# Optimization experiments

Hardware: AMD Instinct MI355X
Metric: run time of the kernel (lower is better)

The kernel has to match this reference:

```python
import jax, jax.numpy as jnp
import numpy as np

HEAD = 8
PAD = (2, 2)   # (mod//2, mod//2 + mod%2) for dim=508, head=8 -> mod=4
EPS = 1e-6


def setup_inputs() -> dict:
    key = jax.random.key(0)
    ks = jax.random.split(key, 4)
    d_pad = 512  # 508 + mod(4)
    s = 1.0 / np.sqrt(d_pad).astype(np.float32)
    inp = jax.random.normal(ks[0], (2, 2048, 508), dtype=jnp.float32)
    Wq = jax.random.normal(ks[1], (d_pad, d_pad), dtype=jnp.float32) * s
    Wk = jax.random.normal(ks[2], (d_pad, d_pad), dtype=jnp.float32) * s
    Wv = jax.random.normal(ks[3], (d_pad, d_pad), dtype=jnp.float32) * s
    gamma = jnp.ones((d_pad,), dtype=jnp.float32)
    beta = jnp.zeros((d_pad,), dtype=jnp.float32)
    return {"inp": inp, "Wq": Wq, "Wk": Wk, "Wv": Wv, "gamma": gamma, "beta": beta}


def reference(inp, Wq, Wk, Wv, gamma, beta):
    # pad feature dim so it divides head count (torch F.pad on last dim)
    x = jnp.pad(inp, ((0, 0), (0, 0), (PAD[0], PAD[1])))  # [B, L, D]
    residual = x
    b, l, d = x.shape
    h = HEAD
    dh = d // h
    inv_sqrt_dh = 1.0 / np.sqrt(dh).astype(np.float32)

    def proj(W):
        # torch Linear (no bias): x @ W.T ; then split heads -> [B, H, L, dh]
        return (x @ W.T).reshape(b, l, h, dh).transpose(0, 2, 1, 3)

    q = proj(Wq)
    k = proj(Wk)
    v = proj(Wv)

    score = jnp.einsum('bhld,bhmd->bhlm', q, k) * inv_sqrt_dh  # [B,H,L,L]
    attn = jax.nn.softmax(score, axis=-1)
    out = jnp.einsum('bhlm,bhmd->bhld', attn, v)               # [B,H,L,dh]
    out = out.transpose(0, 2, 1, 3).reshape(b, l, d)           # unshape

    # dropout is identity in eval mode; residual + layernorm
    y = out + residual
    mu = jnp.mean(y, axis=-1, keepdims=True)
    var = jnp.mean(jnp.square(y - mu), axis=-1, keepdims=True)
    z = (y - mu) / jnp.sqrt(var + EPS)
    out = gamma * z + beta

    out = out[:, :, PAD[0]:-PAD[1]]  # strip padding back to original dim
    return out, attn
```

## Files before the change

kernel.cpp:

```cpp
#include <hip/hip_runtime.h>

typedef short bf16x8 __attribute__((ext_vector_type(8)));
typedef float f32x4 __attribute__((ext_vector_type(4)));
typedef unsigned short u16;
typedef u16 u16x8 __attribute__((ext_vector_type(8)));
typedef u16 u16x4 __attribute__((ext_vector_type(4)));

#define L_ 2048
#define D_ 512
#define H_ 8
#define DH_ 64
#define DIN 508

static __device__ __forceinline__ u16 f2b(float f){
  unsigned u = __builtin_bit_cast(unsigned, f);
  unsigned r = u + 0x7fffu + ((u >> 16) & 1u);
  return (u16)(r >> 16);
}
static __device__ __forceinline__ float b2f(u16 u){
  unsigned x = ((unsigned)u) << 16;
  return __builtin_bit_cast(float, x);
}
#define MFMA16(a,b,c) __builtin_amdgcn_mfma_f32_16x16x32_bf16(a,b,c,0,0,0)

__global__ __launch_bounds__(512) void cvt_kernel(
    const float* __restrict__ inp, const float* __restrict__ Wq,
    const float* __restrict__ Wk, const float* __restrict__ Wv,
    u16* __restrict__ Xb, u16* __restrict__ Wb)
{
  const int tid = blockIdx.x*512 + threadIdx.x;
  if (tid < 262144) {
    const int idx8 = tid*8;
    const int row = idx8 >> 9, col = idx8 & 511;
    u16x8 o;
    #pragma unroll
    for (int e=0;e<8;++e){
      const int c = col+e;
      const float v = (c>=2 && c<510) ? inp[(size_t)row*DIN + (c-2)] : 0.f;
      o[e] = f2b(v);
    }
    *(u16x8*)&Xb[idx8] = o;
  } else {
    const int idx8 = (tid - 262144)*8;
    const int row = idx8 >> 9, col = idx8 & 511;
    const float* __restrict__ W = (row < 512) ? Wq : (row < 1024) ? Wk : Wv;
    const float* p = &W[(size_t)(row & 511)*D_ + col];
    u16x8 o;
    #pragma unroll
    for (int e=0;e<8;++e) o[e] = f2b(p[e]);
    *(u16x8*)&Wb[idx8] = o;
  }
}

__global__ __launch_bounds__(512) void proj_kernel(
    const u16* __restrict__ Xb, const u16* __restrict__ Wb,
    u16* __restrict__ Qg, u16* __restrict__ Kg, u16* __restrict__ Vt)
{
  __shared__ u16 Xl[128*72];
  __shared__ u16 Wl[128*72];
  const int t = threadIdx.x;
  const int lane = t & 63, wid = t >> 6;
  const int wr = wid >> 2, wc = wid & 3;
  const int i0 = blockIdx.x * 128;
  const int j0 = blockIdx.y * 128;
  const int mat = j0 >> 9;
  const int srow = t >> 3, sc8 = (t & 7) * 8;

  f32x4 acc[4][2];
  #pragma unroll
  for (int a=0;a<4;++a){
    #pragma unroll
    for (int bq=0;bq<2;++bq){ f32x4 z = {0.f,0.f,0.f,0.f}; acc[a][bq] = z; }
  }

  u16x8 xa0 = *(const u16x8*)&Xb[(size_t)(i0+srow)*D_ + sc8];
  u16x8 xa1 = *(const u16x8*)&Xb[(size_t)(i0+64+srow)*D_ + sc8];
  u16x8 wa0 = *(const u16x8*)&Wb[(size_t)(j0+srow)*D_ + sc8];
  u16x8 wa1 = *(const u16x8*)&Wb[(size_t)(j0+64+srow)*D_ + sc8];

  for (int kt=0; kt<8; ++kt){
    __syncthreads();
    *(u16x8*)&Xl[srow*72 + sc8] = xa0;
    *(u16x8*)&Xl[(64+srow)*72 + sc8] = xa1;
    *(u16x8*)&Wl[srow*72 + sc8] = wa0;
    *(u16x8*)&Wl[(64+srow)*72 + sc8] = wa1;
    __syncthreads();
    if (kt < 7){
      const int k1 = (kt+1)*64;
      xa0 = *(const u16x8*)&Xb[(size_t)(i0+srow)*D_ + k1 + sc8];
      xa1 = *(const u16x8*)&Xb[(size_t)(i0+64+srow)*D_ + k1 + sc8];
      wa0 = *(const u16x8*)&Wb[(size_t)(j0+srow)*D_ + k1 + sc8];
      wa1 = *(const u16x8*)&Wb[(size_t)(j0+64+srow)*D_ + k1 + sc8];
    }
    #pragma unroll
    for (int ks=0; ks<2; ++ks){
      const int ko = ks*32 + (lane>>4)*8;
      bf16x8 af[4], bfr[2];
      #pragma unroll
      for (int fm=0; fm<4; ++fm)
        af[fm] = *(const bf16x8*)&Xl[(wr*64 + fm*16 + (lane&15))*72 + ko];
      #pragma unroll
      for (int fn=0; fn<2; ++fn)
        bfr[fn] = *(const bf16x8*)&Wl[(wc*32 + fn*16 + (lane&15))*72 + ko];
      #pragma unroll
      for (int fm=0; fm<4; ++fm){
        #pragma unroll
        for (int fn=0; fn<2; ++fn)
          acc[fm][fn] = MFMA16(af[fm], bfr[fn], acc[fm][fn]);
      }
    }
  }
  #pragma unroll
  for (int fm=0; fm<4; ++fm){
    const int ibase = i0 + wr*64 + fm*16 + (lane>>4)*4;
    const int b = ibase >> 11;
    const int li = ibase & (L_-1);
    #pragma unroll
    for (int fn=0; fn<2; ++fn){
      const int n = j0 + wc*32 + fn*16 + (lane&15);
      const int h = (n>>6) & 7;
      const int dh = n & 63;
      if (mat == 2){
        u16x4 pk;
        #pragma unroll
        for (int r=0;r<4;++r) pk[r] = f2b(acc[fm][fn][r]);
        *(u16x4*)&Vt[((size_t)(b*H_+h)*DH_ + dh)*L_ + li] = pk;
      } else {
        u16* dst = ((mat==0)? Qg : Kg) + ((size_t)(b*H_+h)*L_ + li)*DH_ + dh;
        #pragma unroll
        for (int r=0;r<4;++r) dst[(size_t)r*DH_] = f2b(acc[fm][fn][r]);
      }
    }
  }
}

__global__ __launch_bounds__(512, 4) void attn_kernel(
    const u16* __restrict__ Qg, const u16* __restrict__ Kg,
    const u16* __restrict__ Vt, float* __restrict__ attn, float* __restrict__ Og)
{
  __shared__ u16 Kl[128*72];
  __shared__ u16 Vl[64*136];
  __shared__ u16 Pt[32*136];
  __shared__ float rsp[8][32];
  __shared__ float inv_rs[32];

  const int t = threadIdx.x, lane = t & 63, wid = t >> 6;
  const int lin = blockIdx.x;
  const int idx = lin >> 3;
  const int bh = (lin & 7) + 8*(idx & 1);
  const int q0 = (idx >> 1) * 32;
  const u16* Qp = Qg + ((size_t)bh*L_ + q0)*DH_;
  const u16* Kp = Kg + (size_t)bh*L_*DH_;
  const u16* Vp = Vt + (size_t)bh*DH_*L_;

  bf16x8 qf[2][2];
  #pragma unroll
  for (int qi=0;qi<2;++qi){
    #pragma unroll
    for (int ks=0;ks<2;++ks)
      qf[qi][ks] = *(const bf16x8*)&Qp[(size_t)(qi*16 + (lane&15))*DH_ + ks*32 + (lane>>4)*8];
  }

  const int kr0 = t>>3, kc8 = (t&7)*8;
  const int vr0 = t>>4, vcm = (t&15)*8;
  const int g4 = (lane>>4)*8;
  const int mrow = wid*16 + (lane&15);

  float racc0 = 0.f, racc1 = 0.f;
  u16x8 ka = *(const u16x8*)&Kp[(size_t)kr0*DH_ + kc8];
  u16x8 kb = *(const u16x8*)&Kp[(size_t)(64+kr0)*DH_ + kc8];
  for (int kt=0; kt<16; ++kt){
    __syncthreads();
    *(u16x8*)&Kl[kr0*72 + kc8] = ka;
    *(u16x8*)&Kl[(64+kr0)*72 + kc8] = kb;
    __syncthreads();
    if (kt < 15){
      ka = *(const u16x8*)&Kp[(size_t)((kt+1)*128 + kr0)*DH_ + kc8];
      kb = *(const u16x8*)&Kp[(size_t)((kt+1)*128 + 64 + kr0)*DH_ + kc8];
    }
    bf16x8 kf0 = *(const bf16x8*)&Kl[mrow*72 + g4];
    bf16x8 kf1 = *(const bf16x8*)&Kl[mrow*72 + 32 + g4];
    f32x4 s0 = {0.f,0.f,0.f,0.f}, s1 = {0.f,0.f,0.f,0.f};
    s0 = MFMA16(kf0, qf[0][0], s0); s0 = MFMA16(kf1, qf[0][1], s0);
    s1 = MFMA16(kf0, qf[1][0], s1); s1 = MFMA16(kf1, qf[1][1], s1);
    #pragma unroll
    for (int r=0;r<4;++r){
      racc0 += __expf(s0[r]*0.125f);
      racc1 += __expf(s1[r]*0.125f);
    }
  }
  racc0 += __shfl_xor(racc0, 16); racc0 += __shfl_xor(racc0, 32);
  racc1 += __shfl_xor(racc1, 16); racc1 += __shfl_xor(racc1, 32);
  if (lane < 16){ rsp[wid][lane] = racc0; rsp[wid][16+lane] = racc1; }
  __syncthreads();
  if (t < 32){
    float s = 0.f;
    #pragma unroll
    for (int w=0;w<8;++w) s += rsp[w][t];
    inv_rs[t] = 1.f/s;
  }
  __syncthreads();

  const int qpv = wid>>2, d0 = (wid&3)*16;
  f32x4 o0 = {0.f,0.f,0.f,0.f}, o1 = {0.f,0.f,0.f,0.f};
  const int sr = t >> 4;
  const int sc4 = (t & 15) * 4;
  float* abase = attn + ((size_t)bh*L_ + q0 + sr)*L_ + sc4;
  const float sinv = inv_rs[sr];

  ka = *(const u16x8*)&Kp[(size_t)kr0*DH_ + kc8];
  kb = *(const u16x8*)&Kp[(size_t)(64+kr0)*DH_ + kc8];
  u16x8 va = *(const u16x8*)&Vp[(size_t)vr0*L_ + vcm];
  u16x8 vb = *(const u16x8*)&Vp[(size_t)(32+vr0)*L_ + vcm];
  for (int kt=0; kt<16; ++kt){
    __syncthreads();
    *(u16x8*)&Kl[kr0*72 + kc8] = ka;
    *(u16x8*)&Kl[(64+kr0)*72 + kc8] = kb;
    *(u16x8*)&Vl[vr0*136 + vcm] = va;
    *(u16x8*)&Vl[(32+vr0)*136 + vcm] = vb;
    __syncthreads();
    if (kt < 15){
      ka = *(const u16x8*)&Kp[(size_t)((kt+1)*128 + kr0)*DH_ + kc8];
      kb = *(const u16x8*)&Kp[(size_t)((kt+1)*128 + 64 + kr0)*DH_ + kc8];
      va = *(const u16x8*)&Vp[(size_t)vr0*L_ + (kt+1)*128 + vcm];
      vb = *(const u16x8*)&Vp[(size_t)(32+vr0)*L_ + (kt+1)*128 + vcm];
    }
    bf16x8 kf0 = *(const bf16x8*)&Kl[mrow*72 + g4];
    bf16x8 kf1 = *(const bf16x8*)&Kl[mrow*72 + 32 + g4];
    f32x4 s0 = {0.f,0.f,0.f,0.f}, s1 = {0.f,0.f,0.f,0.f};
    s0 = MFMA16(kf0, qf[0][0], s0); s0 = MFMA16(kf1, qf[0][1], s0);
    s1 = MFMA16(kf0, qf[1][0], s1); s1 = MFMA16(kf1, qf[1][1], s1);
    u16x4 p0, p1;
    p0[0] = f2b(__expf(s0[0]*0.125f)); p0[1] = f2b(__expf(s0[1]*0.125f));
    p0[2] = f2b(__expf(s0[2]*0.125f)); p0[3] = f2b(__expf(s0[3]*0.125f));
    p1[0] = f2b(__expf(s1[0]*0.125f)); p1[1] = f2b(__expf(s1[1]*0.125f));
    p1[2] = f2b(__expf(s1[2]*0.125f)); p1[3] = f2b(__expf(s1[3]*0.125f));
    *(u16x4*)&Pt[(lane&15)*136 + wid*16 + (lane>>4)*4] = p0;
    *(u16x4*)&Pt[(16 + (lane&15))*136 + wid*16 + (lane>>4)*4] = p1;
    __syncthreads();
    {
      const u16x4 pva = *(const u16x4*)&Pt[sr*136 + sc4];
      const u16x4 pvb = *(const u16x4*)&Pt[sr*136 + 64 + sc4];
      f32x4 w0, w1;
      w0[0]=b2f(pva[0])*sinv; w0[1]=b2f(pva[1])*sinv;
      w0[2]=b2f(pva[2])*sinv; w0[3]=b2f(pva[3])*sinv;
      w1[0]=b2f(pvb[0])*sinv; w1[1]=b2f(pvb[1])*sinv;
      w1[2]=b2f(pvb[2])*sinv; w1[3]=b2f(pvb[3])*sinv;
      __builtin_nontemporal_store(w0, (f32x4*)&abase[kt*128]);
      __builtin_nontemporal_store(w1, (f32x4*)&abase[kt*128 + 64]);
    }
    #pragma unroll
    for (int ms=0; ms<4; ++ms){
      bf16x8 pa = *(const bf16x8*)&Pt[(qpv*16 + (lane&15))*136 + ms*32 + g4];
      bf16x8 vv = *(const bf16x8*)&Vl[(d0 + (lane&15))*136 + ms*32 + g4];
      if (ms&1) o1 = MFMA16(pa, vv, o1); else o0 = MFMA16(pa, vv, o0);
    }
  }
  {
    const int b = bh>>3, h = bh&7;
    #pragma unroll
    for (int r=0;r<4;++r){
      const int qr = qpv*16 + (lane>>4)*4 + r;
      Og[((size_t)(b*L_ + q0 + qr))*D_ + h*DH_ + d0 + (lane&15)] = (o0[r]+o1[r])*inv_rs[qr];
    }
  }
}

__global__ __launch_bounds__(256) void ln_kernel(
    const float* __restrict__ Og, const float* __restrict__ inp,
    const float* __restrict__ gamma, const float* __restrict__ beta,
    float* __restrict__ out0)
{
  const int row = blockIdx.x, t = threadIdx.x;
  const int lane = t & 63, wid = t >> 6;
  const int c2 = t + 256;
  const float x1 = (t >= 2) ? inp[(size_t)row*DIN + t-2] : 0.f;
  const float x2 = (c2 < 510) ? inp[(size_t)row*DIN + c2-2] : 0.f;
  const float y1 = Og[(size_t)row*D_ + t]  + x1;
  const float y2 = Og[(size_t)row*D_ + c2] + x2;
  float s = y1 + y2, ss = y1*y1 + y2*y2;
  #pragma unroll
  for (int off=1; off<64; off<<=1){
    s  += __shfl_xor(s,  off);
    ss += __shfl_xor(ss, off);
  }
  __shared__ float red[4][2];
  if (lane == 0){ red[wid][0] = s; red[wid][1] = ss; }
  __syncthreads();
  s  = red[0][0]+red[1][0]+red[2][0]+red[3][0];
  ss = red[0][1]+red[1][1]+red[2][1]+red[3][1];
  const float mu   = s * (1.f/512.f);
  const float var  = ss * (1.f/512.f) - mu*mu;
  const float rstd = rsqrtf(var + 1e-6f);
  const float z1 = (y1 - mu)*rstd*gamma[t]  + beta[t];
  const float z2 = (y2 - mu)*rstd*gamma[c2] + beta[c2];
  if (t >= 2)   out0[(size_t)row*DIN + t-2]  = z1;
  if (c2 < 510) out0[(size_t)row*DIN + c2-2] = z2;
}

extern "C" void kernel_launch(void* const* d_in, const int* in_sizes, int n_in,
                              void* d_out, int out_size, void* d_ws, size_t ws_size,
                              hipStream_t stream) {
  const float* inp   = (const float*)d_in[0];
  const float* Wq    = (const float*)d_in[1];
  const float* Wk    = (const float*)d_in[2];
  const float* Wv    = (const float*)d_in[3];
  const float* gamma = (const float*)d_in[4];
  const float* beta  = (const float*)d_in[5];

  char* ws = (char*)d_ws;
  u16*   Qg = (u16*)(ws);
  u16*   Kg = (u16*)(ws + 4194304);
  u16*   Vt = (u16*)(ws + 8388608);
  float* Og = (float*)(ws + 12582912);
  u16*   Xb = (u16*)(ws + 12582912);
  u16*   Wb = (u16*)(ws + 16777216);

  float* out0 = (float*)d_out;
  float* attn = out0 + 2080768;

  cvt_kernel <<<704, 512, 0, stream>>>(inp, Wq, Wk, Wv, Xb, Wb);
  proj_kernel<<<dim3(32,12), 512, 0, stream>>>(Xb, Wb, Qg, Kg, Vt);
  attn_kernel<<<1024, 512, 0, stream>>>(Qg, Kg, Vt, attn, Og);
  ln_kernel  <<<4096, 256, 0, stream>>>(Og, inp, gamma, beta, out0);
}
```

Before: 127.1 us.

## Load K/V fragments straight from global, compute PV in registers, double-buffer P

The attention kernel stops staging K and V through shared memory. Each wave loads its K rows and V^T fragments directly from global memory and feeds them to MFMA. PV is now computed per wave with 16x16x16 MFMAs on the wave's own P fragment, so the P tile no longer needs a round trip through LDS before the PV product, and two syncs per iteration are removed. P is double-buffered in LDS only for writing out the attention matrix. Each wave then holds partial outputs for all 32x64 elements, which must be tree-reduced across 8 waves through shared memory at the end. This raises register pressure and redundant global traffic for V, which each wave reads for its own key slice.

```diff
diff --git a/kernel.cpp b/kernel.cpp
--- a/kernel.cpp
+++ b/kernel.cpp
@@ -1,6 +1,7 @@
 #include <hip/hip_runtime.h>
 
 typedef short bf16x8 __attribute__((ext_vector_type(8)));
+typedef short bf16x4 __attribute__((ext_vector_type(4)));
 typedef float f32x4 __attribute__((ext_vector_type(4)));
 typedef unsigned short u16;
 typedef u16 u16x8 __attribute__((ext_vector_type(8)));
@@ -21,7 +22,30 @@
   unsigned x = ((unsigned)u) << 16;
   return __builtin_bit_cast(float, x);
 }
+static __device__ __forceinline__ bf16x8 asbf(u16x8 v){
+  return __builtin_bit_cast(bf16x8, v);
+}
+static __device__ __forceinline__ bf16x4 asbf4(u16x4 v){
+  return __builtin_bit_cast(bf16x4, v);
+}
 #define MFMA16(a,b,c) __builtin_amdgcn_mfma_f32_16x16x32_bf16(a,b,c,0,0,0)
+
+#if __has_builtin(__builtin_amdgcn_mfma_f32_16x16x16bf16_1k)
+static __device__ __forceinline__ f32x4 MFMA16K16(bf16x4 a, bf16x4 b, f32x4 c){
+  return __builtin_amdgcn_mfma_f32_16x16x16bf16_1k(a, b, c, 0, 0, 0);
+}
+#elif __has_builtin(__builtin_amdgcn_mfma_f32_16x16x16_bf16)
+static __device__ __forceinline__ f32x4 MFMA16K16(bf16x4 a, bf16x4 b, f32x4 c){
+  return __builtin_amdgcn_mfma_f32_16x16x16_bf16(a, b, c, 0, 0, 0);
+}
+#else
+static __device__ __forceinline__ f32x4 MFMA16K16(bf16x4 a, bf16x4 b, f32x4 c){
+  f32x4 d;
+  asm volatile("v_mfma_f32_16x16x16_bf16 %0, %1, %2, %3\n\ts_nop 7"
+               : "=&v"(d) : "v"(a), "v"(b), "v"(c));
+  return d;
+}
+#endif
 
 __global__ __launch_bounds__(512) void cvt_kernel(
     const float* __restrict__ inp, const float* __restrict__ Wq,
@@ -138,13 +162,15 @@
     const u16* __restrict__ Qg, const u16* __restrict__ Kg,
     const u16* __restrict__ Vt, float* __restrict__ attn, float* __restrict__ Og)
 {
-  __shared__ u16 Kl[128*72];
-  __shared__ u16 Vl[64*136];
-  __shared__ u16 Pt[32*136];
-  __shared__ float rsp[8][32];
-  __shared__ float inv_rs[32];
+  __shared__ char smem[35968];
+  u16*   Pt0    = (u16*)smem;
+  u16*   Pt1    = (u16*)(smem + 8704);
+  float* red    = (float*)smem;
+  float* rsp    = (float*)(smem + 34816);
+  float* inv_rs = (float*)(smem + 35840);
 
   const int t = threadIdx.x, lane = t & 63, wid = t >> 6;
+  const int lane15 = lane & 15, g = lane >> 4;
   const int lin = blockIdx.x;
   const int idx = lin >> 3;
   const int bh = (lin & 7) + 8*(idx & 1);
@@ -158,89 +184,90 @@
   for (int qi=0;qi<2;++qi){
     #pragma unroll
     for (int ks=0;ks<2;++ks)
-      qf[qi][ks] = *(const bf16x8*)&Qp[(size_t)(qi*16 + (lane&15))*DH_ + ks*32 + (lane>>4)*8];
-  }
-
-  const int kr0 = t>>3, kc8 = (t&7)*8;
-  const int vr0 = t>>4, vcm = (t&15)*8;
-  const int g4 = (lane>>4)*8;
-  const int mrow = wid*16 + (lane&15);
+      qf[qi][ks] = *(const bf16x8*)&Qp[(size_t)(qi*16 + lane15)*DH_ + ks*32 + g*8];
+  }
+
+  const int g4 = g*8;
+  const int mrow = wid*16 + lane15;
 
   float racc0 = 0.f, racc1 = 0.f;
-  u16x8 ka = *(const u16x8*)&Kp[(size_t)kr0*DH_ + kc8];
-  u16x8 kb = *(const u16x8*)&Kp[(size_t)(64+kr0)*DH_ + kc8];
-  for (int kt=0; kt<16; ++kt){
-    __syncthreads();
-    *(u16x8*)&Kl[kr0*72 + kc8] = ka;
-    *(u16x8*)&Kl[(64+kr0)*72 + kc8] = kb;
-    __syncthreads();
-    if (kt < 15){
-      ka = *(const u16x8*)&Kp[(size_t)((kt+1)*128 + kr0)*DH_ + kc8];
-      kb = *(const u16x8*)&Kp[(size_t)((kt+1)*128 + 64 + kr0)*DH_ + kc8];
-    }
-    bf16x8 kf0 = *(const bf16x8*)&Kl[mrow*72 + g4];
-    bf16x8 kf1 = *(const bf16x8*)&Kl[mrow*72 + 32 + g4];
-    f32x4 s0 = {0.f,0.f,0.f,0.f}, s1 = {0.f,0.f,0.f,0.f};
-    s0 = MFMA16(kf0, qf[0][0], s0); s0 = MFMA16(kf1, qf[0][1], s0);
-    s1 = MFMA16(kf0, qf[1][0], s1); s1 = MFMA16(kf1, qf[1][1], s1);
-    #pragma unroll
-    for (int r=0;r<4;++r){
-      racc0 += __expf(s0[r]*0.125f);
-      racc1 += __expf(s1[r]*0.125f);
+  {
+    u16x8 nk0 = *(const u16x8*)&Kp[(size_t)mrow*DH_ + g4];
+    u16x8 nk1 = *(const u16x8*)&Kp[(size_t)mrow*DH_ + 32 + g4];
+    for (int kt=0; kt<16; ++kt){
+      bf16x8 kf0 = asbf(nk0), kf1 = asbf(nk1);
+      if (kt < 15){
+        nk0 = *(const u16x8*)&Kp[(size_t)((kt+1)*128 + mrow)*DH_ + g4];
+        nk1 = *(const u16x8*)&Kp[(size_t)((kt+1)*128 + mrow)*DH_ + 32 + g4];
+      }
+      f32x4 s0 = {0.f,0.f,0.f,0.f}, s1 = {0.f,0.f,0.f,0.f};
+      s0 = MFMA16(kf0, qf[0][0], s0); s0 = MFMA16(kf1, qf[0][1], s0);
+      s1 = MFMA16(kf0, qf[1][0], s1); s1 = MFMA16(kf1, qf[1][1], s1);
+      #pragma unroll
+      for (int r=0;r<4;++r){
+        racc0 += __expf(s0[r]*0.125f);
+        racc1 += __expf(s1[r]*0.125f);
+      }
     }
   }
   racc0 += __shfl_xor(racc0, 16); racc0 += __shfl_xor(racc0, 32);
   racc1 += __shfl_xor(racc1, 16); racc1 += __shfl_xor(racc1, 32);
-  if (lane < 16){ rsp[wid][lane] = racc0; rsp[wid][16+lane] = racc1; }
+  if (lane < 16){ rsp[wid*32 + lane] = racc0; rsp[wid*32 + 16 + lane] = racc1; }
   __syncthreads();
   if (t < 32){
     float s = 0.f;
     #pragma unroll
-    for (int w=0;w<8;++w) s += rsp[w][t];
+    for (int w=0;w<8;++w) s += rsp[w*32 + t];
     inv_rs[t] = 1.f/s;
   }
   __syncthreads();
 
-  const int qpv = wid>>2, d0 = (wid&3)*16;
-  f32x4 o0 = {0.f,0.f,0.f,0.f}, o1 = {0.f,0.f,0.f,0.f};
+  f32x4 o[2][4];
+  #pragma unroll
+  for (int qi=0;qi<2;++qi){
+    #pragma unroll
+    for (int db=0;db<4;++db){ f32x4 z = {0.f,0.f,0.f,0.f}; o[qi][db] = z; }
+  }
   const int sr = t >> 4;
   const int sc4 = (t & 15) * 4;
   float* abase = attn + ((size_t)bh*L_ + q0 + sr)*L_ + sc4;
   const float sinv = inv_rs[sr];
 
-  ka = *(const u16x8*)&Kp[(size_t)kr0*DH_ + kc8];
-  kb = *(const u16x8*)&Kp[(size_t)(64+kr0)*DH_ + kc8];
-  u16x8 va = *(const u16x8*)&Vp[(size_t)vr0*L_ + vcm];
-  u16x8 vb = *(const u16x8*)&Vp[(size_t)(32+vr0)*L_ + vcm];
+  u16x8 k0 = *(const u16x8*)&Kp[(size_t)mrow*DH_ + g4];
+  u16x8 k1 = *(const u16x8*)&Kp[(size_t)mrow*DH_ + 32 + g4];
   for (int kt=0; kt<16; ++kt){
-    __syncthreads();
-    *(u16x8*)&Kl[kr0*72 + kc8] = ka;
-    *(u16x8*)&Kl[(64+kr0)*72 + kc8] = kb;
-    *(u16x8*)&Vl[vr0*136 + vcm] = va;
-    *(u16x8*)&Vl[(32+vr0)*136 + vcm] = vb;
-    __syncthreads();
+    u16* Ptc = (kt & 1) ? Pt1 : Pt0;
+    const int m0w = kt*128 + wid*16 + g*4;
+    bf16x4 vf0 = *(const bf16x4*)&Vp[(size_t)( 0 + lane15)*L_ + m0w];
+    bf16x4 vf1 = *(const bf16x4*)&Vp[(size_t)(16 + lane15)*L_ + m0w];
+    bf16x4 vf2 = *(const bf16x4*)&Vp[(size_t)(32 + lane15)*L_ + m0w];
+    bf16x4 vf3 = *(const bf16x4*)&Vp[(size_t)(48 + lane15)*L_ + m0w];
+    f32x4 s0 = {0.f,0.f,0.f,0.f}, s1 = {0.f,0.f,0.f,0.f};
+    s0 = MFMA16(asbf(k0), qf[0][0], s0); s0 = MFMA16(asbf(k1), qf[0][1], s0);
+    s1 = MFMA16(asbf(k0), qf[1][0], s1); s1 = MFMA16(asbf(k1), qf[1][1], s1);
     if (kt < 15){
-      ka = *(const u16x8*)&Kp[(size_t)((kt+1)*128 + kr0)*DH_ + kc8];
-      kb = *(const u16x8*)&Kp[(size_t)((kt+1)*128 + 64 + kr0)*DH_ + kc8];
-      va = *(const u16x8*)&Vp[(size_t)vr0*L_ + (kt+1)*128 + vcm];
-      vb = *(const u16x8*)&Vp[(size_t)(32+vr0)*L_ + (kt+1)*128 + vcm];
-    }
-    bf16x8 kf0 = *(const bf16x8*)&Kl[mrow*72 + g4];
-    bf16x8 kf1 = *(const bf16x8*)&Kl[mrow*72 + 32 + g4];
-    f32x4 s0 = {0.f,0.f,0.f,0.f}, s1 = {0.f,0.f,0.f,0.f};
-    s0 = MFMA16(kf0, qf[0][0], s0); s0 = MFMA16(kf1, qf[0][1], s0);
-    s1 = MFMA16(kf0, qf[1][0], s1); s1 = MFMA16(kf1, qf[1][1], s1);
+      k0 = *(const u16x8*)&Kp[(size_t)((kt+1)*128 + mrow)*DH_ + g4];
+      k1 = *(const u16x8*)&Kp[(size_t)((kt+1)*128 + mrow)*DH_ + 32 + g4];
+    }
     u16x4 p0, p1;
     p0[0] = f2b(__expf(s0[0]*0.125f)); p0[1] = f2b(__expf(s0[1]*0.125f));
     p0[2] = f2b(__expf(s0[2]*0.125f)); p0[3] = f2b(__expf(s0[3]*0.125f));
     p1[0] = f2b(__expf(s1[0]*0.125f)); p1[1] = f2b(__expf(s1[1]*0.125f));
     p1[2] = f2b(__expf(s1[2]*0.125f)); p1[3] = f2b(__expf(s1[3]*0.125f));
-    *(u16x4*)&Pt[(lane&15)*136 + wid*16 + (lane>>4)*4] = p0;
-    *(u16x4*)&Pt[(16 + (lane&15))*136 + wid*16 + (lane>>4)*4] = p1;
+    *(u16x4*)&Ptc[lane15*136 + wid*16 + g*4] = p0;
+    *(u16x4*)&Ptc[(16 + lane15)*136 + wid*16 + g*4] = p1;
+    o[0][0] = MFMA16K16(asbf4(p0), vf0, o[0][0]);
+    o[1][0] = MFMA16K16(asbf4(p1), vf0, o[1][0]);
+    o[0][1] = MFMA16K16(asbf4(p0), vf1, o[0][1]);
+    o[1][1] = MFMA16K16(asbf4(p1), vf1, o[1][1]);
+    o[0][2] = MFMA16K16(asbf4(p0), vf2, o[0][2]);
+    o[1][2] = MFMA16K16(asbf4(p1), vf2, o[1][2]);
+    o[0][3] = MFMA16K16(asbf4(p0), vf3, o[0][3]);
+    o[1][3] = MFMA16K16(asbf4(p1), vf3, o[1][3]);
     __syncthreads();
     {
-      const u16x4 pva = *(const u16x4*)&Pt[sr*136 + sc4];
-      const u16x4 pvb = *(const u16x4*)&Pt[sr*136 + 64 + sc4];
+      const u16x4 pva = *(const u16x4*)&Ptc[sr*136 + sc4];
+      const u16x4 pvb = *(const u16x4*)&Ptc[sr*136 + 64 + sc4];
       f32x4 w0, w1;
       w0[0]=b2f(pva[0])*sinv; w0[1]=b2f(pva[1])*sinv;
       w0[2]=b2f(pva[2])*sinv; w0[3]=b2f(pva[3])*sinv;
@@ -249,20 +276,50 @@
       __builtin_nontemporal_store(w0, (f32x4*)&abase[kt*128]);
       __builtin_nontemporal_store(w1, (f32x4*)&abase[kt*128 + 64]);
     }
-    #pragma unroll
-    for (int ms=0; ms<4; ++ms){
-      bf16x8 pa = *(const bf16x8*)&Pt[(qpv*16 + (lane&15))*136 + ms*32 + g4];
-      bf16x8 vv = *(const bf16x8*)&Vl[(d0 + (lane&15))*136 + ms*32 + g4];
-      if (ms&1) o1 = MFMA16(pa, vv, o1); else o0 = MFMA16(pa, vv, o0);
-    }
-  }
+  }
+
+  __syncthreads();
+  if (wid < 4){
+    #pragma unroll
+    for (int qi=0;qi<2;++qi)
+      #pragma unroll
+      for (int db=0;db<4;++db)
+        #pragma unroll
+        for (int r=0;r<4;++r)
+          red[wid*2176 + (qi*16 + g*4 + r)*68 + db*16 + lane15] = o[qi][db][r];
+  }
+  __syncthreads();
+  if (wid >= 4){
+    #pragma unroll
+    for (int qi=0;qi<2;++qi)
+      #pragma unroll
+      for (int db=0;db<4;++db)
+        #pragma unroll
+        for (int r=0;r<4;++r)
+          red[(wid-4)*2176 + (qi*16 + g*4 + r)*68 + db*16 + lane15] += o[qi][db][r];
+  }
+  __syncthreads();
+  if (wid < 2){
+    for (int j=0; j<32; ++j){
+      const int q = (j*64 + lane) >> 6, d = (j*64 + lane) & 63;
+      red[wid*2176 + q*68 + d] += red[(wid+2)*2176 + q*68 + d];
+    }
+  }
+  __syncthreads();
+  if (wid == 0){
+    for (int j=0; j<32; ++j){
+      const int q = (j*64 + lane) >> 6, d = (j*64 + lane) & 63;
+      red[q*68 + d] += red[2176 + q*68 + d];
+    }
+  }
+  __syncthreads();
   {
     const int b = bh>>3, h = bh&7;
-    #pragma unroll
-    for (int r=0;r<4;++r){
-      const int qr = qpv*16 + (lane>>4)*4 + r;
-      Og[((size_t)(b*L_ + q0 + qr))*D_ + h*DH_ + d0 + (lane&15)] = (o0[r]+o1[r])*inv_rs[qr];
-    }
+    const int qq = t >> 4, dc = (t & 15)*4;
+    const float iv = inv_rs[qq];
+    f32x4 vv = *(const f32x4*)&red[qq*68 + dc];
+    vv[0]*=iv; vv[1]*=iv; vv[2]*=iv; vv[3]*=iv;
+    *(f32x4*)&Og[((size_t)(b*L_ + q0 + qq))*D_ + h*DH_ + dc] = vv;
   }
 }
 
```

New measurement: 163.4 us. 1.28x slower.

## Split softmax row-sum pass into separate kernel with larger Q tiles

Applied to the files above, without the earlier changes.

Moves the first pass (QK^T exp row-sum) out of the attention kernel into a dedicated rowsum kernel. It handles 64 query rows per block and reads K fragments directly from global memory without LDS or barriers. The attention kernel then loads precomputed inverse row sums and only does the second pass. Its occupancy hint rises to 6 blocks. The cost is an extra kernel launch and a small global buffer, with K read again in the second kernel.

```diff
diff --git a/kernel.cpp b/kernel.cpp
--- a/kernel.cpp
+++ b/kernel.cpp
@@ -20,6 +20,9 @@
 static __device__ __forceinline__ float b2f(u16 u){
   unsigned x = ((unsigned)u) << 16;
   return __builtin_bit_cast(float, x);
+}
+static __device__ __forceinline__ bf16x8 asbf(u16x8 v){
+  return __builtin_bit_cast(bf16x8, v);
 }
 #define MFMA16(a,b,c) __builtin_amdgcn_mfma_f32_16x16x32_bf16(a,b,c,0,0,0)
 
@@ -134,15 +137,73 @@
   }
 }
 
-__global__ __launch_bounds__(512, 4) void attn_kernel(
+__global__ __launch_bounds__(512, 4) void rowsum_kernel(
     const u16* __restrict__ Qg, const u16* __restrict__ Kg,
-    const u16* __restrict__ Vt, float* __restrict__ attn, float* __restrict__ Og)
+    float* __restrict__ rsg)
+{
+  __shared__ float rsp[8][64];
+  const int t = threadIdx.x, lane = t & 63, wid = t >> 6;
+  const int lane15 = lane & 15, g4 = (lane >> 4) * 8;
+  const int lin = blockIdx.x;
+  const int bh = (lin & 7) + 8*((lin >> 3) & 1);
+  const int q0 = (lin >> 4) * 64;
+  const u16* Qp = Qg + ((size_t)bh*L_ + q0)*DH_;
+  const u16* Kp = Kg + (size_t)bh*L_*DH_;
+  const int mrow = wid*16 + lane15;
+
+  bf16x8 qf[4][2];
+  #pragma unroll
+  for (int qi=0;qi<4;++qi){
+    #pragma unroll
+    for (int ks=0;ks<2;++ks)
+      qf[qi][ks] = *(const bf16x8*)&Qp[(size_t)(qi*16 + lane15)*DH_ + ks*32 + g4];
+  }
+
+  float racc[4] = {0.f, 0.f, 0.f, 0.f};
+  u16x8 nk0 = *(const u16x8*)&Kp[(size_t)mrow*DH_ + g4];
+  u16x8 nk1 = *(const u16x8*)&Kp[(size_t)mrow*DH_ + 32 + g4];
+  for (int kt=0; kt<16; ++kt){
+    bf16x8 kf0 = asbf(nk0), kf1 = asbf(nk1);
+    if (kt < 15){
+      nk0 = *(const u16x8*)&Kp[(size_t)((kt+1)*128 + mrow)*DH_ + g4];
+      nk1 = *(const u16x8*)&Kp[(size_t)((kt+1)*128 + mrow)*DH_ + 32 + g4];
+    }
+    #pragma unroll
+    for (int qi=0;qi<4;++qi){
+      f32x4 s = {0.f,0.f,0.f,0.f};
+      s = MFMA16(kf0, qf[qi][0], s);
+      s = MFMA16(kf1, qf[qi][1], s);
+      #pragma unroll
+      for (int r=0;r<4;++r) racc[qi] += __expf(s[r]*0.125f);
+    }
+  }
+  #pragma unroll
+  for (int qi=0;qi<4;++qi){
+    racc[qi] += __shfl_xor(racc[qi], 16);
+    racc[qi] += __shfl_xor(racc[qi], 32);
+  }
+  if (lane < 16){
+    #pragma unroll
+    for (int qi=0;qi<4;++qi) rsp[wid][qi*16 + lane] = racc[qi];
+  }
+  __syncthreads();
+  if (t < 64){
+    float s = 0.f;
+    #pragma unroll
+    for (int w=0;w<8;++w) s += rsp[w][t];
+    rsg[(size_t)bh*L_ + q0 + t] = 1.f/s;
+  }
+}
+
+__global__ __launch_bounds__(512, 6) void attn_kernel(
+    const u16* __restrict__ Qg, const u16* __restrict__ Kg,
+    const u16* __restrict__ Vt, const float* __restrict__ rsg,
+    float* __restrict__ attn, float* __restrict__ Og)
 {
   __shared__ u16 Kl[128*72];
   __shared__ u16 Vl[64*136];
   __shared__ u16 Pt[32*136];
-  __shared__ float rsp[8][32];
-  __shared__ float inv_rs[32];
+  __shared__ float inv_lds[32];
 
   const int t = threadIdx.x, lane = t & 63, wid = t >> 6;
   const int lin = blockIdx.x;
@@ -153,6 +214,8 @@
   const u16* Kp = Kg + (size_t)bh*L_*DH_;
   const u16* Vp = Vt + (size_t)bh*DH_*L_;
 
+  if (t < 32) inv_lds[t] = rsg[(size_t)bh*L_ + q0 + t];
+
   bf16x8 qf[2][2];
   #pragma unroll
   for (int qi=0;qi<2;++qi){
@@ -165,53 +228,21 @@
   const int vr0 = t>>4, vcm = (t&15)*8;
   const int g4 = (lane>>4)*8;
   const int mrow = wid*16 + (lane&15);
-
-  float racc0 = 0.f, racc1 = 0.f;
-  u16x8 ka = *(const u16x8*)&Kp[(size_t)kr0*DH_ + kc8];
-  u16x8 kb = *(const u16x8*)&Kp[(size_t)(64+kr0)*DH_ + kc8];
-  for (int kt=0; kt<16; ++kt){
-    __syncthreads();
-    *(u16x8*)&Kl[kr0*72 + kc8] = ka;
-    *(u16x8*)&Kl[(64+kr0)*72 + kc8] = kb;
-    __syncthreads();
-    if (kt < 15){
-      ka = *(const u16x8*)&Kp[(size_t)((kt+1)*128 + kr0)*DH_ + kc8];
-      kb = *(const u16x8*)&Kp[(size_t)((kt+1)*128 + 64 + kr0)*DH_ + kc8];
-    }
-    bf16x8 kf0 = *(const bf16x8*)&Kl[mrow*72 + g4];
-    bf16x8 kf1 = *(const bf16x8*)&Kl[mrow*72 + 32 + g4];
-    f32x4 s0 = {0.f,0.f,0.f,0.f}, s1 = {0.f,0.f,0.f,0.f};
-    s0 = MFMA16(kf0, qf[0][0], s0); s0 = MFMA16(kf1, qf[0][1], s0);
-    s1 = MFMA16(kf0, qf[1][0], s1); s1 = MFMA16(kf1, qf[1][1], s1);
-    #pragma unroll
-    for (int r=0;r<4;++r){
-      racc0 += __expf(s0[r]*0.125f);
-      racc1 += __expf(s1[r]*0.125f);
-    }
-  }
-  racc0 += __shfl_xor(racc0, 16); racc0 += __shfl_xor(racc0, 32);
-  racc1 += __shfl_xor(racc1, 16); racc1 += __shfl_xor(racc1, 32);
-  if (lane < 16){ rsp[wid][lane] = racc0; rsp[wid][16+lane] = racc1; }
-  __syncthreads();
-  if (t < 32){
-    float s = 0.f;
-    #pragma unroll
-    for (int w=0;w<8;++w) s += rsp[w][t];
-    inv_rs[t] = 1.f/s;
-  }
-  __syncthreads();
 
   const int qpv = wid>>2, d0 = (wid&3)*16;
   f32x4 o0 = {0.f,0.f,0.f,0.f}, o1 = {0.f,0.f,0.f,0.f};
   const int sr = t >> 4;
   const int sc4 = (t & 15) * 4;
   float* abase = attn + ((size_t)bh*L_ + q0 + sr)*L_ + sc4;
-  const float sinv = inv_rs[sr];
-
-  ka = *(const u16x8*)&Kp[(size_t)kr0*DH_ + kc8];
-  kb = *(const u16x8*)&Kp[(size_t)(64+kr0)*DH_ + kc8];
+
+  u16x8 ka = *(const u16x8*)&Kp[(size_t)kr0*DH_ + kc8];
+  u16x8 kb = *(const u16x8*)&Kp[(size_t)(64+kr0)*DH_ + kc8];
   u16x8 va = *(const u16x8*)&Vp[(size_t)vr0*L_ + vcm];
   u16x8 vb = *(const u16x8*)&Vp[(size_t)(32+vr0)*L_ + vcm];
+
+  __syncthreads();
+  const float sinv = inv_lds[sr];
+
   for (int kt=0; kt<16; ++kt){
     __syncthreads();
     *(u16x8*)&Kl[kr0*72 + kc8] = ka;
@@ -261,7 +292,7 @@
     #pragma unroll
     for (int r=0;r<4;++r){
       const int qr = qpv*16 + (lane>>4)*4 + r;
-      Og[((size_t)(b*L_ + q0 + qr))*D_ + h*DH_ + d0 + (lane&15)] = (o0[r]+o1[r])*inv_rs[qr];
+      Og[((size_t)(b*L_ + q0 + qr))*D_ + h*DH_ + d0 + (lane&15)] = (o0[r]+o1[r])*inv_lds[qr];
     }
   }
 }
@@ -309,18 +340,20 @@
   const float* beta  = (const float*)d_in[5];
 
   char* ws = (char*)d_ws;
-  u16*   Qg = (u16*)(ws);
-  u16*   Kg = (u16*)(ws + 4194304);
-  u16*   Vt = (u16*)(ws + 8388608);
-  float* Og = (float*)(ws + 12582912);
-  u16*   Xb = (u16*)(ws + 12582912);
-  u16*   Wb = (u16*)(ws + 16777216);
+  u16*   Qg  = (u16*)(ws);
+  u16*   Kg  = (u16*)(ws + 4194304);
+  u16*   Vt  = (u16*)(ws + 8388608);
+  float* Og  = (float*)(ws + 12582912);
+  u16*   Xb  = (u16*)(ws + 12582912);
+  u16*   Wb  = (u16*)(ws + 16777216);
+  float* rsg = (float*)(ws + 20971520);
 
   float* out0 = (float*)d_out;
   float* attn = out0 + 2080768;
 
-  cvt_kernel <<<704, 512, 0, stream>>>(inp, Wq, Wk, Wv, Xb, Wb);
-  proj_kernel<<<dim3(32,12), 512, 0, stream>>>(Xb, Wb, Qg, Kg, Vt);
-  attn_kernel<<<1024, 512, 0, stream>>>(Qg, Kg, Vt, attn, Og);
-  ln_kernel  <<<4096, 256, 0, stream>>>(Og, inp, gamma, beta, out0);
-}
+  cvt_kernel   <<<704, 512, 0, stream>>>(inp, Wq, Wk, Wv, Xb, Wb);
+  proj_kernel  <<<dim3(32,12), 512, 0, stream>>>(Xb, Wb, Qg, Kg, Vt);
+  rowsum_kernel<<<512, 512, 0, stream>>>(Qg, Kg, rsg);
+  attn_kernel  <<<1024, 512, 0, stream>>>(Qg, Kg, Vt, rsg, attn, Og);
+  ln_kernel    <<<4096, 256, 0, stream>>>(Og, inp, gamma, beta, out0);
+}
```

Measured after the change: 135.7 us. 6.7% more time.

## Load projection GEMM tiles directly into LDS with larger per-wave tiles

Applied to the files above, without the earlier changes.

The QKV projection kernel now issues 16-byte global-to-LDS loads (global_load_lds) instead of staging tiles through registers. It also drops to 256 threads, with each of the four waves computing a 64x64 output tile instead of 64x32. This is meant to cut register staging and VGPR use and to raise MFMA work per LDS fragment load. In exchange, the register prefetch of the next K tile is gone, so load latency is no longer overlapped. The LDS row padding is also removed, which can cause bank conflicts on fragment reads.

```diff
diff --git a/kernel.cpp b/kernel.cpp
--- a/kernel.cpp
+++ b/kernel.cpp
@@ -21,7 +21,16 @@
   unsigned x = ((unsigned)u) << 16;
   return __builtin_bit_cast(float, x);
 }
+static __device__ __forceinline__ bf16x8 asbf(u16x8 v){
+  return __builtin_bit_cast(bf16x8, v);
+}
 #define MFMA16(a,b,c) __builtin_amdgcn_mfma_f32_16x16x32_bf16(a,b,c,0,0,0)
+
+static __device__ __forceinline__ void async16(u16* lds, const u16* g){
+  __builtin_amdgcn_global_load_lds(
+      (const __attribute__((address_space(1))) unsigned int*)g,
+      (__attribute__((address_space(3))) unsigned int*)lds, 16, 0, 0);
+}
 
 __global__ __launch_bounds__(512) void cvt_kernel(
     const float* __restrict__ inp, const float* __restrict__ Wq,
@@ -52,72 +61,64 @@
   }
 }
 
-__global__ __launch_bounds__(512) void proj_kernel(
+__global__ __launch_bounds__(256) void proj_kernel(
     const u16* __restrict__ Xb, const u16* __restrict__ Wb,
     u16* __restrict__ Qg, u16* __restrict__ Kg, u16* __restrict__ Vt)
 {
-  __shared__ u16 Xl[128*72];
-  __shared__ u16 Wl[128*72];
+  __shared__ u16 Al[128*64];
+  __shared__ u16 Bl[128*64];
   const int t = threadIdx.x;
   const int lane = t & 63, wid = t >> 6;
-  const int wr = wid >> 2, wc = wid & 3;
+  const int lane15 = lane & 15, g = lane >> 4, g4 = g*8;
+  const int wr = wid >> 1, wc = wid & 1;
   const int i0 = blockIdx.x * 128;
   const int j0 = blockIdx.y * 128;
   const int mat = j0 >> 9;
-  const int srow = t >> 3, sc8 = (t & 7) * 8;
-
-  f32x4 acc[4][2];
+  const int srow = wid*32 + (lane >> 3);
+  const int scol = (lane & 7) * 8;
+
+  f32x4 acc[4][4];
   #pragma unroll
   for (int a=0;a<4;++a){
     #pragma unroll
-    for (int bq=0;bq<2;++bq){ f32x4 z = {0.f,0.f,0.f,0.f}; acc[a][bq] = z; }
-  }
-
-  u16x8 xa0 = *(const u16x8*)&Xb[(size_t)(i0+srow)*D_ + sc8];
-  u16x8 xa1 = *(const u16x8*)&Xb[(size_t)(i0+64+srow)*D_ + sc8];
-  u16x8 wa0 = *(const u16x8*)&Wb[(size_t)(j0+srow)*D_ + sc8];
-  u16x8 wa1 = *(const u16x8*)&Wb[(size_t)(j0+64+srow)*D_ + sc8];
+    for (int bq=0;bq<4;++bq){ f32x4 z = {0.f,0.f,0.f,0.f}; acc[a][bq] = z; }
+  }
 
   for (int kt=0; kt<8; ++kt){
-    __syncthreads();
-    *(u16x8*)&Xl[srow*72 + sc8] = xa0;
-    *(u16x8*)&Xl[(64+srow)*72 + sc8] = xa1;
-    *(u16x8*)&Wl[srow*72 + sc8] = wa0;
-    *(u16x8*)&Wl[(64+srow)*72 + sc8] = wa1;
-    __syncthreads();
-    if (kt < 7){
-      const int k1 = (kt+1)*64;
-      xa0 = *(const u16x8*)&Xb[(size_t)(i0+srow)*D_ + k1 + sc8];
-      xa1 = *(const u16x8*)&Xb[(size_t)(i0+64+srow)*D_ + k1 + sc8];
-      wa0 = *(const u16x8*)&Wb[(size_t)(j0+srow)*D_ + k1 + sc8];
-      wa1 = *(const u16x8*)&Wb[(size_t)(j0+64+srow)*D_ + k1 + sc8];
-    }
+    const int k0 = kt*64;
+    __syncthreads();
+    #pragma unroll
+    for (int j=0;j<4;++j){
+      async16(&Al[wid*2048 + j*512], &Xb[(size_t)(i0 + srow + j*8)*D_ + k0 + scol]);
+      async16(&Bl[wid*2048 + j*512], &Wb[(size_t)(j0 + srow + j*8)*D_ + k0 + scol]);
+    }
+    __syncthreads();
     #pragma unroll
     for (int ks=0; ks<2; ++ks){
-      const int ko = ks*32 + (lane>>4)*8;
-      bf16x8 af[4], bfr[2];
+      const int ko = ks*32 + g4;
+      bf16x8 af[4], bfr[4];
       #pragma unroll
       for (int fm=0; fm<4; ++fm)
-        af[fm] = *(const bf16x8*)&Xl[(wr*64 + fm*16 + (lane&15))*72 + ko];
+        af[fm] = *(const bf16x8*)&Al[(wr*64 + fm*16 + lane15)*64 + ko];
       #pragma unroll
-      for (int fn=0; fn<2; ++fn)
-        bfr[fn] = *(const bf16x8*)&Wl[(wc*32 + fn*16 + (lane&15))*72 + ko];
+      for (int fn=0; fn<4; ++fn)
+        bfr[fn] = *(const bf16x8*)&Bl[(wc*64 + fn*16 + lane15)*64 + ko];
       #pragma unroll
       for (int fm=0; fm<4; ++fm){
         #pragma unroll
-        for (int fn=0; fn<2; ++fn)
+        for (int fn=0; fn<4; ++fn)
           acc[fm][fn] = MFMA16(af[fm], bfr[fn], acc[fm][fn]);
       }
     }
   }
   #pragma unroll
   for (int fm=0; fm<4; ++fm){
-    const int ibase = i0 + wr*64 + fm*16 + (lane>>4)*4;
+    const int ibase = i0 + wr*64 + fm*16 + g*4;
     const int b = ibase >> 11;
     const int li = ibase & (L_-1);
     #pragma unroll
-    for (int fn=0; fn<2; ++fn){
-      const int n = j0 + wc*32 + fn*16 + (lane&15);
+    for (int fn=0; fn<4; ++fn){
+      const int n = j0 + wc*64 + fn*16 + lane15;
       const int h = (n>>6) & 7;
       const int dh = n & 63;
       if (mat == 2){
@@ -320,7 +321,7 @@
   float* attn = out0 + 2080768;
 
   cvt_kernel <<<704, 512, 0, stream>>>(inp, Wq, Wk, Wv, Xb, Wb);
-  proj_kernel<<<dim3(32,12), 512, 0, stream>>>(Xb, Wb, Qg, Kg, Vt);
+  proj_kernel<<<dim3(32,12), 256, 0, stream>>>(Xb, Wb, Qg, Kg, Vt);
   attn_kernel<<<1024, 512, 0, stream>>>(Qg, Kg, Vt, attn, Og);
   ln_kernel  <<<4096, 256, 0, stream>>>(Og, inp, gamma, beta, out0);
 }
```

Measured after the change: 128.7 us. About the same (+1.2%).
